# Kernel tuning notes

Measured on AMD Instinct MI355X. Metric: run time of the kernel, lower is better.

The kernel has to match this reference:

```python
import jax, jax.numpy as jnp
import numpy as np

N = 20000
E = 640000
D = 128      # node_dim
R = 32       # rbf_dim
H = 128      # radial_hidden_dim
CUTOFF = 5.0
RES_SCALE_INIT = 0.1
LN_EPS = 1e-5


def _init_linear(key, fan_in, fan_out):
    kw, kb = jax.random.split(key)
    bound = 1.0 / np.sqrt(fan_in)
    w = jax.random.uniform(kw, (fan_in, fan_out), minval=-bound, maxval=bound, dtype=jnp.float32)
    b = jax.random.uniform(kb, (fan_out,), minval=-bound, maxval=bound, dtype=jnp.float32)
    return w, b


def setup_inputs() -> dict:
    key = jax.random.key(0)
    ks = jax.random.split(key, 16)
    x = jax.random.normal(ks[0], (N, D), dtype=jnp.float32)
    edge_src = jax.random.randint(ks[1], (E,), 0, N)
    edge_dst = jax.random.randint(ks[2], (E,), 0, N)
    edge_sh = jax.random.normal(ks[3], (E, 16), dtype=jnp.float32)
    edge_rbf = jax.random.uniform(ks[4], (E, R), dtype=jnp.float32)
    edge_len = jax.random.uniform(ks[5], (E,), dtype=jnp.float32) * 8.0  # some edges beyond cutoff

    wm_w1, wm_b1 = _init_linear(ks[6], R, H)
    wm_w2, wm_b2 = _init_linear(ks[7], H, H)
    wm_w3, wm_b3 = _init_linear(ks[8], H, D)
    eg_w1, eg_b1 = _init_linear(ks[9], R, H)
    eg_w2, eg_b2 = _init_linear(ks[10], H, 1)
    mm_w1, mm_b1 = _init_linear(ks[11], D, H)
    mm_w2, mm_b2 = _init_linear(ks[12], H, D)
    sl_w, sl_b = _init_linear(ks[13], D, D)
    ul_w, ul_b = _init_linear(ks[14], D, D)

    return {
        "x": x, "edge_src": edge_src, "edge_dst": edge_dst,
        "edge_sh": edge_sh, "edge_rbf": edge_rbf, "edge_len": edge_len,
        "ln_g": jnp.ones((D,), jnp.float32), "ln_b": jnp.zeros((D,), jnp.float32),
        "wm_w1": wm_w1, "wm_b1": wm_b1, "wm_w2": wm_w2, "wm_b2": wm_b2,
        "wm_w3": wm_w3, "wm_b3": wm_b3,
        "eg_w1": eg_w1, "eg_b1": eg_b1, "eg_w2": eg_w2, "eg_b2": eg_b2,
        "mm_w1": mm_w1, "mm_b1": mm_b1, "mm_w2": mm_w2, "mm_b2": mm_b2,
        "sl_w": sl_w, "sl_b": sl_b, "ul_w": ul_w, "ul_b": ul_b,
        "res_scale": jnp.float32(RES_SCALE_INIT),
    }


def reference(x, edge_src, edge_dst, edge_sh, edge_rbf, edge_len,
              ln_g, ln_b,
              wm_w1, wm_b1, wm_w2, wm_b2, wm_w3, wm_b3,
              eg_w1, eg_b1, eg_w2, eg_b2,
              mm_w1, mm_b1, mm_w2, mm_b2,
              sl_w, sl_b, ul_w, ul_b, res_scale):
    # pre-LayerNorm
    mu = jnp.mean(x, axis=-1, keepdims=True)
    var = jnp.var(x, axis=-1, keepdims=True)
    x_norm = (x - mu) * jax.lax.rsqrt(var + LN_EPS) * ln_g + ln_b  # [N, D]

    # cosine cutoff * sigmoid edge gate -> [E, 1]
    r = edge_len / CUTOFF
    cut = 0.5 * (jnp.cos(jnp.pi * r) + 1.0) * (edge_len <= CUTOFF).astype(x.dtype)
    g = jax.nn.silu(edge_rbf @ eg_w1 + eg_b1)
    gate = jax.nn.sigmoid(g @ eg_w2 + eg_b2)  # [E, 1]
    edge_w = cut[:, None] * gate               # [E, 1]

    # radial weight MLP [E, D]
    h = jax.nn.silu(edge_rbf @ wm_w1 + wm_b1)
    h = jax.nn.silu(h @ wm_w2 + wm_b2)
    w_rad = h @ wm_w3 + wm_b3

    # gather, gate, scatter-add
    m = x_norm[edge_src] * w_rad * edge_w       # [E, D]
    agg = jax.ops.segment_sum(m, edge_dst, num_segments=N)          # [N, D]
    norm = jax.ops.segment_sum(edge_w, edge_dst, num_segments=N)    # [N, 1]
    agg = agg / jnp.maximum(norm, 1e-8)

    # message MLP + update
    a = jax.nn.silu(agg @ mm_w1 + mm_b1)
    agg2 = a @ mm_w2 + mm_b2
    out = (x_norm @ sl_w + sl_b) + (agg2 @ ul_w + ul_b)
    return x + res_scale * out
```

## Files before the change

### kernel.cpp

```cpp
#include <hip/hip_runtime.h>
#include <math.h>

#define N_NODES 20000
#define N_EDGES 640000
#define DD 128
#define RR 32
#define HH 128
#define PI_F 3.14159265358979323846f

#define NPACK 416
#define NLN   5000
#define NHIST 2500

typedef short bf16x8 __attribute__((ext_vector_type(8)));
typedef float f32x4 __attribute__((ext_vector_type(4)));
typedef __bf16 bf16x2_t __attribute__((ext_vector_type(2)));

__device__ __forceinline__ float silu_f(float x) {
    return x * __builtin_amdgcn_rcpf(1.0f + __expf(-x));
}
__device__ __forceinline__ float sigmoid_f(float x) {
    return __builtin_amdgcn_rcpf(1.0f + __expf(-x));
}
__device__ __forceinline__ unsigned short f2bf(float x) {
    __bf16 h = (__bf16)x;
    return __builtin_bit_cast(unsigned short, h);
}
__device__ __forceinline__ unsigned pk2(float lo, float hi) {
    bf16x2_t v;
    v[0] = (__bf16)lo; v[1] = (__bf16)hi;
    return __builtin_bit_cast(unsigned, v);
}
__device__ __forceinline__ bf16x8 frag8(float4 a, float4 b) {
    union { unsigned u[4]; bf16x8 v; } r;
    r.u[0] = pk2(a.x, a.y); r.u[1] = pk2(a.z, a.w);
    r.u[2] = pk2(b.x, b.y); r.u[3] = pk2(b.z, b.w);
    return r.v;
}

__device__ __forceinline__ unsigned short pack_one(const float* __restrict__ src,
                                                   int o, int F) {
    int NT = F >> 4;
    int j = o & 7;
    int l = (o >> 3) & 63;
    int rest = o >> 9;
    int t = rest % NT;
    int s = rest / NT;
    int k = s * 32 + ((l >> 4) << 3) + j;
    int f = t * 16 + (l & 15);
    return f2bf(src[(size_t)k * F + f]);
}

__global__ __launch_bounds__(256) void prep_kernel(
    const float* __restrict__ eg_w1, const float* __restrict__ wm_w1,
    const float* __restrict__ wm_w2, const float* __restrict__ wm_w3,
    const float* __restrict__ mm_w1, const float* __restrict__ mm_w2,
    const float* __restrict__ sl_w,  const float* __restrict__ ul_w,
    unsigned short* __restrict__ wp,
    const float* __restrict__ x, const float* __restrict__ g,
    const float* __restrict__ b, float* __restrict__ xn,
    const int* __restrict__ edst, const float* __restrict__ elen,
    int* __restrict__ cnt)
{
    const int blk = blockIdx.x;
    if (blk < NPACK) {
        int o = blk * 256 + threadIdx.x;
        unsigned short v;
        if      (o < 4096)   v = pack_one(eg_w1, o,          HH);
        else if (o < 8192)   v = pack_one(wm_w1, o - 4096,   HH);
        else if (o < 24576)  v = pack_one(wm_w2, o - 8192,   HH);
        else if (o < 40960)  v = pack_one(wm_w3, o - 24576,  DD);
        else if (o < 57344)  v = pack_one(mm_w1, o - 40960,  HH);
        else if (o < 73728)  v = pack_one(mm_w2, o - 57344,  DD);
        else if (o < 90112)  v = pack_one(sl_w,  o - 73728,  DD);
        else                 v = pack_one(ul_w,  o - 90112,  DD);
        wp[o] = v;
    } else if (blk < NPACK + NLN) {
        int wid = ((blk - NPACK) * 256 + threadIdx.x) >> 6;
        int lane = threadIdx.x & 63;
        if (wid >= N_NODES) return;
        const float* row = x + (size_t)wid * DD;
        float v0 = row[lane], v1 = row[lane + 64];
        float s = v0 + v1, sq = v0 * v0 + v1 * v1;
        #pragma unroll
        for (int o = 32; o > 0; o >>= 1) { s += __shfl_xor(s, o); sq += __shfl_xor(sq, o); }
        float mu = s * (1.0f / 128.0f);
        float var = sq * (1.0f / 128.0f) - mu * mu;
        float inv = rsqrtf(var + 1e-5f);
        float* orow = xn + (size_t)wid * DD;
        orow[lane]      = (v0 - mu) * inv * g[lane]      + b[lane];
        orow[lane + 64] = (v1 - mu) * inv * g[lane + 64] + b[lane + 64];
    } else {
        int e = (blk - NPACK - NLN) * 256 + threadIdx.x;
        if (e < N_EDGES && elen[e] <= 5.0f) atomicAdd(&cnt[edst[e]], 1);
    }
}

__global__ __launch_bounds__(1024) void scan_kernel(const int* __restrict__ cnt,
                                                    int* __restrict__ offs,
                                                    int* __restrict__ cursor) {
    __shared__ int part[1024];
    const int t = threadIdx.x;
    const int per = 20;
    const int base = t * per;
    int s = 0;
    for (int i = 0; i < per; ++i) {
        int idx = base + i;
        if (idx < N_NODES) s += cnt[idx];
    }
    part[t] = s;
    __syncthreads();
    for (int off = 1; off < 1024; off <<= 1) {
        int v = (t >= off) ? part[t - off] : 0;
        __syncthreads();
        part[t] += v;
        __syncthreads();
    }
    int run = part[t] - s;
    for (int i = 0; i < per; ++i) {
        int idx = base + i;
        if (idx < N_NODES) {
            offs[idx] = run;
            cursor[idx] = run;
            run += cnt[idx];
        }
    }
    if (t == 1023) offs[N_NODES] = part[1023];
}

__global__ __launch_bounds__(256) void fill_kernel(const int* __restrict__ esrc,
                                                   const int* __restrict__ edst,
                                                   const float* __restrict__ elen,
                                                   int* __restrict__ cursor,
                                                   int4* __restrict__ erec) {
    int e = blockIdx.x * 256 + threadIdx.x;
    if (e >= N_EDGES) return;
    float len = elen[e];
    if (len <= 5.0f) {
        int d = edst[e];
        int pos = atomicAdd(&cursor[d], 1);
        float cut = 0.5f * (__cosf(PI_F * len * 0.2f) + 1.0f);
        int4 rec;
        rec.x = e;
        rec.y = esrc[e];
        rec.z = d;
        rec.w = __float_as_int(cut);
        erec[pos] = rec;
    }
}

__global__ __launch_bounds__(256, 4) void edge_seg_kernel(
    const float* __restrict__ xn,
    const float* __restrict__ rbf,
    const int4* __restrict__ erec, const int* __restrict__ nlive_p,
    const unsigned short* __restrict__ wp_eg1, const unsigned short* __restrict__ wp_w1,
    const unsigned short* __restrict__ wp_w2,  const unsigned short* __restrict__ wp_w3,
    const float* __restrict__ eg_b1, const float* __restrict__ eg_w2,
    const float* __restrict__ eg_b2,
    const float* __restrict__ wm_b1, const float* __restrict__ wm_b2,
    const float* __restrict__ wm_b3,
    float* __restrict__ agg, float* __restrict__ nrm)
{
    __shared__ unsigned short act[4][32 * 136];
    __shared__ float ew_s[128];
    __shared__ int   dst_s[128];

    const int nlive = nlive_p[0];
    if (blockIdx.x * 128 >= nlive) return;

    const int tid  = threadIdx.x;
    const int w    = tid >> 6;
    const int lane = tid & 63;
    const int er   = lane & 15;
    const int kq   = lane >> 4;

    const int g0 = blockIdx.x * 128 + w * 32 + er;
    const int g1 = g0 + 16;
    const bool v0 = g0 < nlive, v1 = g1 < nlive;
    const int4 r0 = erec[v0 ? g0 : nlive - 1];
    const int4 r1 = erec[v1 ? g1 : nlive - 1];

    const int e0 = r0.x, src0 = r0.y, dst0 = r0.z;
    const int e1 = r1.x, src1 = r1.y, dst1 = r1.z;
    const float cut0 = v0 ? __int_as_float(r0.w) : 0.0f;
    const float cut1 = v1 ? __int_as_float(r1.w) : 0.0f;

    const float4* rp = (const float4*)(rbf + (size_t)e0 * RR + kq * 8);
    bf16x8 bfr0 = frag8(rp[0], rp[1]);
    const float4* rq = (const float4*)(rbf + (size_t)e1 * RR + kq * 8);
    bf16x8 bfr1 = frag8(rq[0], rq[1]);

    unsigned short* buf = &act[w][0];

    float pd0 = 0.0f, pd1 = 0.0f;
    {
        bf16x8 agc = *(const bf16x8*)(wp_eg1 + (size_t)lane * 8);
        bf16x8 a1c = *(const bf16x8*)(wp_w1  + (size_t)lane * 8);
        #pragma unroll
        for (int t = 0; t < 8; ++t) {
            const int tn = (t + 1) & 7;
            bf16x8 agn = *(const bf16x8*)(wp_eg1 + ((size_t)tn * 64 + lane) * 8);
            bf16x8 a1n = *(const bf16x8*)(wp_w1  + ((size_t)tn * 64 + lane) * 8);
            float4 gb = *(const float4*)(eg_b1 + t * 16 + kq * 4);
            float4 b1 = *(const float4*)(wm_b1 + t * 16 + kq * 4);
            f32x4 cg0 = {gb.x, gb.y, gb.z, gb.w};
            f32x4 cg1 = cg0;
            f32x4 c10 = {b1.x, b1.y, b1.z, b1.w};
            f32x4 c11 = c10;
            cg0 = __builtin_amdgcn_mfma_f32_16x16x32_bf16(agc, bfr0, cg0, 0, 0, 0);
            cg1 = __builtin_amdgcn_mfma_f32_16x16x32_bf16(agc, bfr1, cg1, 0, 0, 0);
            c10 = __builtin_amdgcn_mfma_f32_16x16x32_bf16(a1c, bfr0, c10, 0, 0, 0);
            c11 = __builtin_amdgcn_mfma_f32_16x16x32_bf16(a1c, bfr1, c11, 0, 0, 0);
            float4 w2 = *(const float4*)(eg_w2 + t * 16 + kq * 4);
            pd0 += silu_f(cg0[0])*w2.x + silu_f(cg0[1])*w2.y
                 + silu_f(cg0[2])*w2.z + silu_f(cg0[3])*w2.w;
            pd1 += silu_f(cg1[0])*w2.x + silu_f(cg1[1])*w2.y
                 + silu_f(cg1[2])*w2.z + silu_f(cg1[3])*w2.w;
            *(uint2*)(buf + er * 136 + t * 16 + kq * 4) =
                make_uint2(pk2(silu_f(c10[0]), silu_f(c10[1])),
                           pk2(silu_f(c10[2]), silu_f(c10[3])));
            *(uint2*)(buf + (16 + er) * 136 + t * 16 + kq * 4) =
                make_uint2(pk2(silu_f(c11[0]), silu_f(c11[1])),
                           pk2(silu_f(c11[2]), silu_f(c11[3])));
            agc = agn; a1c = a1n;
        }
    }
    pd0 += __shfl_xor(pd0, 16); pd0 += __shfl_xor(pd0, 32);
    pd1 += __shfl_xor(pd1, 16); pd1 += __shfl_xor(pd1, 32);
    const float eb2 = eg_b2[0];
    const float ew0 = cut0 * sigmoid_f(pd0 + eb2);
    const float ew1 = cut1 * sigmoid_f(pd1 + eb2);
    if (lane < 16) {
        ew_s[w * 32 + er] = ew0;       dst_s[w * 32 + er] = dst0;
        ew_s[w * 32 + 16 + er] = ew1;  dst_s[w * 32 + 16 + er] = dst1;
    }

    bf16x8 h0[4], h1[4];
    #pragma unroll
    for (int s = 0; s < 4; ++s) {
        h0[s] = *(const bf16x8*)(buf + er * 136 + s * 32 + kq * 8);
        h1[s] = *(const bf16x8*)(buf + (16 + er) * 136 + s * 32 + kq * 8);
    }
    {
        bf16x8 afc[4];
        #pragma unroll
        for (int s = 0; s < 4; ++s)
            afc[s] = *(const bf16x8*)(wp_w2 + ((size_t)(s * 8) * 64 + lane) * 8);
        #pragma unroll
        for (int t = 0; t < 8; ++t) {
            const int tn = (t + 1) & 7;
            bf16x8 afn[4];
            #pragma unroll
            for (int s = 0; s < 4; ++s)
                afn[s] = *(const bf16x8*)(wp_w2 + (((size_t)s * 8 + tn) * 64 + lane) * 8);
            float4 b2 = *(const float4*)(wm_b2 + t * 16 + kq * 4);
            f32x4 a0 = {b2.x, b2.y, b2.z, b2.w}, b0 = {0.f, 0.f, 0.f, 0.f};
            f32x4 a1 = a0, b1v = {0.f, 0.f, 0.f, 0.f};
            a0 = __builtin_amdgcn_mfma_f32_16x16x32_bf16(afc[0], h0[0], a0, 0, 0, 0);
            b0 = __builtin_amdgcn_mfma_f32_16x16x32_bf16(afc[2], h0[2], b0, 0, 0, 0);
            a1 = __builtin_amdgcn_mfma_f32_16x16x32_bf16(afc[0], h1[0], a1, 0, 0, 0);
            b1v = __builtin_amdgcn_mfma_f32_16x16x32_bf16(afc[2], h1[2], b1v, 0, 0, 0);
            a0 = __builtin_amdgcn_mfma_f32_16x16x32_bf16(afc[1], h0[1], a0, 0, 0, 0);
            b0 = __builtin_amdgcn_mfma_f32_16x16x32_bf16(afc[3], h0[3], b0, 0, 0, 0);
            a1 = __builtin_amdgcn_mfma_f32_16x16x32_bf16(afc[1], h1[1], a1, 0, 0, 0);
            b1v = __builtin_amdgcn_mfma_f32_16x16x32_bf16(afc[3], h1[3], b1v, 0, 0, 0);
            f32x4 c0 = a0 + b0;
            f32x4 c1 = a1 + b1v;
            *(uint2*)(buf + er * 136 + t * 16 + kq * 4) =
                make_uint2(pk2(silu_f(c0[0]), silu_f(c0[1])),
                           pk2(silu_f(c0[2]), silu_f(c0[3])));
            *(uint2*)(buf + (16 + er) * 136 + t * 16 + kq * 4) =
                make_uint2(pk2(silu_f(c1[0]), silu_f(c1[1])),
                           pk2(silu_f(c1[2]), silu_f(c1[3])));
            #pragma unroll
            for (int s = 0; s < 4; ++s) afc[s] = afn[s];
        }
    }

    #pragma unroll
    for (int s = 0; s < 4; ++s) {
        h0[s] = *(const bf16x8*)(buf + er * 136 + s * 32 + kq * 8);
        h1[s] = *(const bf16x8*)(buf + (16 + er) * 136 + s * 32 + kq * 8);
    }
    const float* xr0 = xn + (size_t)src0 * DD;
    const float* xr1 = xn + (size_t)src1 * DD;
    {
        bf16x8 afc[4];
        #pragma unroll
        for (int s = 0; s < 4; ++s)
            afc[s] = *(const bf16x8*)(wp_w3 + ((size_t)(s * 8) * 64 + lane) * 8);
        #pragma unroll
        for (int t = 0; t < 8; ++t) {
            const int tn = (t + 1) & 7;
            bf16x8 afn[4];
            #pragma unroll
            for (int s = 0; s < 4; ++s)
                afn[s] = *(const bf16x8*)(wp_w3 + (((size_t)s * 8 + tn) * 64 + lane) * 8);
            float4 b3 = *(const float4*)(wm_b3 + t * 16 + kq * 4);
            f32x4 a0 = {b3.x, b3.y, b3.z, b3.w}, b0 = {0.f, 0.f, 0.f, 0.f};
            f32x4 a1 = a0, b1v = {0.f, 0.f, 0.f, 0.f};
            a0 = __builtin_amdgcn_mfma_f32_16x16x32_bf16(afc[0], h0[0], a0, 0, 0, 0);
            b0 = __builtin_amdgcn_mfma_f32_16x16x32_bf16(afc[2], h0[2], b0, 0, 0, 0);
            a1 = __builtin_amdgcn_mfma_f32_16x16x32_bf16(afc[0], h1[0], a1, 0, 0, 0);
            b1v = __builtin_amdgcn_mfma_f32_16x16x32_bf16(afc[2], h1[2], b1v, 0, 0, 0);
            a0 = __builtin_amdgcn_mfma_f32_16x16x32_bf16(afc[1], h0[1], a0, 0, 0, 0);
            b0 = __builtin_amdgcn_mfma_f32_16x16x32_bf16(afc[3], h0[3], b0, 0, 0, 0);
            a1 = __builtin_amdgcn_mfma_f32_16x16x32_bf16(afc[1], h1[1], a1, 0, 0, 0);
            b1v = __builtin_amdgcn_mfma_f32_16x16x32_bf16(afc[3], h1[3], b1v, 0, 0, 0);
            f32x4 c0 = a0 + b0;
            f32x4 c1 = a1 + b1v;
            float4 xv0 = *(const float4*)(xr0 + t * 16 + kq * 4);
            float4 xv1 = *(const float4*)(xr1 + t * 16 + kq * 4);
            *(uint2*)(buf + er * 136 + t * 16 + kq * 4) =
                make_uint2(pk2(c0[0]*xv0.x*ew0, c0[1]*xv0.y*ew0),
                           pk2(c0[2]*xv0.z*ew0, c0[3]*xv0.w*ew0));
            *(uint2*)(buf + (16 + er) * 136 + t * 16 + kq * 4) =
                make_uint2(pk2(c1[0]*xv1.x*ew1, c1[1]*xv1.y*ew1),
                           pk2(c1[2]*xv1.z*ew1, c1[3]*xv1.w*ew1));
            #pragma unroll
            for (int s = 0; s < 4; ++s) afc[s] = afn[s];
        }
    }

    {
        const int rb = w * 32;
        float run0 = 0.0f, run1 = 0.0f, ewrun = 0.0f;
        int cur = dst_s[rb];
        #pragma unroll 8
        for (int i = 0; i < 32; ++i) {
            const int d = dst_s[rb + i];
            if (d != cur) {
                atomicAdd(&agg[(size_t)cur * DD + 2 * lane], run0);
                atomicAdd(&agg[(size_t)cur * DD + 2 * lane + 1], run1);
                if (lane == 0) atomicAdd(&nrm[cur], ewrun);
                run0 = 0.0f; run1 = 0.0f; ewrun = 0.0f; cur = d;
            }
            unsigned pv = *(const unsigned*)(buf + i * 136 + 2 * lane);
            run0 += __uint_as_float(pv << 16);
            run1 += __uint_as_float(pv & 0xffff0000u);
            ewrun += ew_s[rb + i];
        }
        atomicAdd(&agg[(size_t)cur * DD + 2 * lane], run0);
        atomicAdd(&agg[(size_t)cur * DD + 2 * lane + 1], run1);
        if (lane == 0) atomicAdd(&nrm[cur], ewrun);
    }
}

__global__ __launch_bounds__(256) void node_kernel(
    const float* __restrict__ x, const float* __restrict__ xn,
    const float* __restrict__ agg, const float* __restrict__ nrm,
    const unsigned short* __restrict__ wp_mm1, const unsigned short* __restrict__ wp_mm2,
    const unsigned short* __restrict__ wp_sl,  const unsigned short* __restrict__ wp_ul,
    const float* __restrict__ mm_b1, const float* __restrict__ mm_b2,
    const float* __restrict__ sl_b, const float* __restrict__ ul_b,
    const float* __restrict__ res_scale, float* __restrict__ out)
{
    __shared__ unsigned short act[4][16 * 136];

    const int tid  = threadIdx.x;
    const int w    = tid >> 6;
    const int lane = tid & 63;
    const int er   = lane & 15;
    const int kq   = lane >> 4;

    const int n0 = blockIdx.x * 64 + w * 16 + er;
    const bool val0 = n0 < N_NODES;
    const int nc0 = val0 ? n0 : N_NODES - 1;

    const float rs0 = __builtin_amdgcn_rcpf(fmaxf(nrm[nc0], 1e-8f));
    const float rscl = res_scale[0];

    bf16x8 ba0[4];
    #pragma unroll
    for (int s = 0; s < 4; ++s) {
        const float4* ap = (const float4*)(agg + (size_t)nc0 * DD + s * 32 + kq * 8);
        float4 a = ap[0], b = ap[1];
        a.x*=rs0; a.y*=rs0; a.z*=rs0; a.w*=rs0; b.x*=rs0; b.y*=rs0; b.z*=rs0; b.w*=rs0;
        ba0[s] = frag8(a, b);
    }

    unsigned short* buf = &act[w][0];

    #pragma unroll
    for (int t = 0; t < 8; ++t) {
        float4 b1 = *(const float4*)(mm_b1 + t * 16 + kq * 4);
        f32x4 c0 = {b1.x, b1.y, b1.z, b1.w};
        #pragma unroll
        for (int s = 0; s < 4; ++s) {
            bf16x8 af = *(const bf16x8*)(wp_mm1 + (((size_t)s * 8 + t) * 64 + lane) * 8);
            c0 = __builtin_amdgcn_mfma_f32_16x16x32_bf16(af, ba0[s], c0, 0, 0, 0);
        }
        *(uint2*)(buf + er * 136 + t * 16 + kq * 4) =
            make_uint2(pk2(silu_f(c0[0]), silu_f(c0[1])),
                       pk2(silu_f(c0[2]), silu_f(c0[3])));
    }

    bf16x8 bh0[4];
    #pragma unroll
    for (int s = 0; s < 4; ++s)
        bh0[s] = *(const bf16x8*)(buf + er * 136 + s * 32 + kq * 8);
    #pragma unroll
    for (int t = 0; t < 8; ++t) {
        float4 b2 = *(const float4*)(mm_b2 + t * 16 + kq * 4);
        f32x4 c0 = {b2.x, b2.y, b2.z, b2.w};
        #pragma unroll
        for (int s = 0; s < 4; ++s) {
            bf16x8 af = *(const bf16x8*)(wp_mm2 + (((size_t)s * 8 + t) * 64 + lane) * 8);
            c0 = __builtin_amdgcn_mfma_f32_16x16x32_bf16(af, bh0[s], c0, 0, 0, 0);
        }
        *(uint2*)(buf + er * 136 + t * 16 + kq * 4) =
            make_uint2(pk2(c0[0], c0[1]), pk2(c0[2], c0[3]));
    }

    bf16x8 bg0[4], bx0[4];
    #pragma unroll
    for (int s = 0; s < 4; ++s) {
        bg0[s] = *(const bf16x8*)(buf + er * 136 + s * 32 + kq * 8);
        const float4* xp = (const float4*)(xn + (size_t)nc0 * DD + s * 32 + kq * 8);
        bx0[s] = frag8(xp[0], xp[1]);
    }

    #pragma unroll
    for (int t = 0; t < 8; ++t) {
        float4 sb = *(const float4*)(sl_b + t * 16 + kq * 4);
        float4 ub = *(const float4*)(ul_b + t * 16 + kq * 4);
        f32x4 c0 = {sb.x + ub.x, sb.y + ub.y, sb.z + ub.z, sb.w + ub.w};
        #pragma unroll
        for (int s = 0; s < 4; ++s) {
            bf16x8 af = *(const bf16x8*)(wp_sl + (((size_t)s * 8 + t) * 64 + lane) * 8);
            c0 = __builtin_amdgcn_mfma_f32_16x16x32_bf16(af, bx0[s], c0, 0, 0, 0);
        }
        #pragma unroll
        for (int s = 0; s < 4; ++s) {
            bf16x8 af = *(const bf16x8*)(wp_ul + (((size_t)s * 8 + t) * 64 + lane) * 8);
            c0 = __builtin_amdgcn_mfma_f32_16x16x32_bf16(af, bg0[s], c0, 0, 0, 0);
        }
        if (val0) {
            float4 xv = *(const float4*)(x + (size_t)n0 * DD + t * 16 + kq * 4);
            float4 o;
            o.x = xv.x + rscl * c0[0];
            o.y = xv.y + rscl * c0[1];
            o.z = xv.z + rscl * c0[2];
            o.w = xv.w + rscl * c0[3];
            *(float4*)(out + (size_t)n0 * DD + t * 16 + kq * 4) = o;
        }
    }
}

extern "C" void kernel_launch(void* const* d_in, const int* in_sizes, int n_in,
                              void* d_out, int out_size, void* d_ws, size_t ws_size,
                              hipStream_t stream) {
    const float* x     = (const float*)d_in[0];
    const int*   esrc  = (const int*)d_in[1];
    const int*   edst  = (const int*)d_in[2];
    const float* rbf   = (const float*)d_in[4];
    const float* elen  = (const float*)d_in[5];
    const float* ln_g  = (const float*)d_in[6];
    const float* ln_b  = (const float*)d_in[7];
    const float* wm_w1 = (const float*)d_in[8];
    const float* wm_b1 = (const float*)d_in[9];
    const float* wm_w2 = (const float*)d_in[10];
    const float* wm_b2 = (const float*)d_in[11];
    const float* wm_w3 = (const float*)d_in[12];
    const float* wm_b3 = (const float*)d_in[13];
    const float* eg_w1 = (const float*)d_in[14];
    const float* eg_b1 = (const float*)d_in[15];
    const float* eg_w2 = (const float*)d_in[16];
    const float* eg_b2 = (const float*)d_in[17];
    const float* mm_w1 = (const float*)d_in[18];
    const float* mm_b1 = (const float*)d_in[19];
    const float* mm_w2 = (const float*)d_in[20];
    const float* mm_b2 = (const float*)d_in[21];
    const float* sl_w  = (const float*)d_in[22];
    const float* sl_b  = (const float*)d_in[23];
    const float* ul_w  = (const float*)d_in[24];
    const float* ul_b  = (const float*)d_in[25];
    const float* rscl  = (const float*)d_in[26];

    float* xn  = (float*)d_ws;
    float* agg = xn + (size_t)N_NODES * DD;
    float* nrm = agg + (size_t)N_NODES * DD;
    int*   cnt = (int*)(nrm + N_NODES);
    unsigned short* wp = (unsigned short*)(cnt + N_NODES);
    unsigned short* wp_eg1 = wp;
    unsigned short* wp_w1  = wp + 4096;
    unsigned short* wp_w2  = wp + 8192;
    unsigned short* wp_w3  = wp + 24576;
    unsigned short* wp_mm1 = wp + 40960;
    unsigned short* wp_mm2 = wp + 57344;
    unsigned short* wp_sl  = wp + 73728;
    unsigned short* wp_ul  = wp + 90112;
    int* offs   = (int*)(wp + 106496);
    int* cursor = offs + N_NODES + 1;
    int4* erec  = (int4*)(((size_t)(cursor + N_NODES) + 15) & ~(size_t)15);

    hipMemsetAsync(agg, 0, (size_t)(N_NODES * DD + 2 * N_NODES) * sizeof(float), stream);
    prep_kernel<<<NPACK + NLN + NHIST, 256, 0, stream>>>(
        eg_w1, wm_w1, wm_w2, wm_w3, mm_w1, mm_w2, sl_w, ul_w, wp,
        x, ln_g, ln_b, xn, edst, elen, cnt);
    scan_kernel<<<1, 1024, 0, stream>>>(cnt, offs, cursor);
    fill_kernel<<<N_EDGES / 256, 256, 0, stream>>>(esrc, edst, elen, cursor, erec);
    edge_seg_kernel<<<N_EDGES / 128, 256, 0, stream>>>(xn, rbf, erec, offs + N_NODES,
        wp_eg1, wp_w1, wp_w2, wp_w3,
        eg_b1, eg_w2, eg_b2, wm_b1, wm_b2, wm_b3, agg, nrm);
    node_kernel<<<(N_NODES + 63) / 64, 256, 0, stream>>>(x, xn, agg, nrm,
        wp_mm1, wp_mm2, wp_sl, wp_ul,
        mm_b1, mm_b2, sl_b, ul_b, rscl, (float*)d_out);
}
```

Before: 204.9 us.

## Fold agg zeroing into prep kernel and software-pipeline node-kernel weight loads

```diff
diff --git a/kernel.cpp b/kernel.cpp
--- a/kernel.cpp
+++ b/kernel.cpp
@@ -11,6 +11,7 @@
 #define NPACK 416
 #define NLN   5000
 #define NHIST 2500
+#define NZERO 2520
 
 typedef short bf16x8 __attribute__((ext_vector_type(8)));
 typedef float f32x4 __attribute__((ext_vector_type(4)));
@@ -60,7 +61,7 @@
     const float* __restrict__ x, const float* __restrict__ g,
     const float* __restrict__ b, float* __restrict__ xn,
     const int* __restrict__ edst, const float* __restrict__ elen,
-    int* __restrict__ cnt)
+    int* __restrict__ cnt, float4* __restrict__ aggz)
 {
     const int blk = blockIdx.x;
     if (blk < NPACK) {
@@ -90,9 +91,13 @@
         float* orow = xn + (size_t)wid * DD;
         orow[lane]      = (v0 - mu) * inv * g[lane]      + b[lane];
         orow[lane + 64] = (v1 - mu) * inv * g[lane + 64] + b[lane + 64];
-    } else {
+    } else if (blk < NPACK + NLN + NHIST) {
         int e = (blk - NPACK - NLN) * 256 + threadIdx.x;
         if (e < N_EDGES && elen[e] <= 5.0f) atomicAdd(&cnt[edst[e]], 1);
+    } else {
+        int i = (blk - NPACK - NLN - NHIST) * 256 + threadIdx.x;
+        if (i < (N_NODES * DD + N_NODES) / 4)
+            aggz[i] = make_float4(0.f, 0.f, 0.f, 0.f);
     }
 }
 
@@ -381,35 +386,61 @@
 
     unsigned short* buf = &act[w][0];
 
-    #pragma unroll
-    for (int t = 0; t < 8; ++t) {
-        float4 b1 = *(const float4*)(mm_b1 + t * 16 + kq * 4);
-        f32x4 c0 = {b1.x, b1.y, b1.z, b1.w};
-        #pragma unroll
-        for (int s = 0; s < 4; ++s) {
-            bf16x8 af = *(const bf16x8*)(wp_mm1 + (((size_t)s * 8 + t) * 64 + lane) * 8);
-            c0 = __builtin_amdgcn_mfma_f32_16x16x32_bf16(af, ba0[s], c0, 0, 0, 0);
-        }
-        *(uint2*)(buf + er * 136 + t * 16 + kq * 4) =
-            make_uint2(pk2(silu_f(c0[0]), silu_f(c0[1])),
-                       pk2(silu_f(c0[2]), silu_f(c0[3])));
+    {
+        bf16x8 afc[4];
+        #pragma unroll
+        for (int s = 0; s < 4; ++s)
+            afc[s] = *(const bf16x8*)(wp_mm1 + ((size_t)(s * 8) * 64 + lane) * 8);
+        #pragma unroll
+        for (int t = 0; t < 8; ++t) {
+            const int tn = (t + 1) & 7;
+            bf16x8 afn[4];
+            #pragma unroll
+            for (int s = 0; s < 4; ++s)
+                afn[s] = *(const bf16x8*)(wp_mm1 + (((size_t)s * 8 + tn) * 64 + lane) * 8);
+            float4 b1 = *(const float4*)(mm_b1 + t * 16 + kq * 4);
+            f32x4 ca = {b1.x, b1.y, b1.z, b1.w}, cb = {0.f, 0.f, 0.f, 0.f};
+            ca = __builtin_amdgcn_mfma_f32_16x16x32_bf16(afc[0], ba0[0], ca, 0, 0, 0);
+            cb = __builtin_amdgcn_mfma_f32_16x16x32_bf16(afc[2], ba0[2], cb, 0, 0, 0);
+            ca = __builtin_amdgcn_mfma_f32_16x16x32_bf16(afc[1], ba0[1], ca, 0, 0, 0);
+            cb = __builtin_amdgcn_mfma_f32_16x16x32_bf16(afc[3], ba0[3], cb, 0, 0, 0);
+            f32x4 c0 = ca + cb;
+            *(uint2*)(buf + er * 136 + t * 16 + kq * 4) =
+                make_uint2(pk2(silu_f(c0[0]), silu_f(c0[1])),
+                           pk2(silu_f(c0[2]), silu_f(c0[3])));
+            #pragma unroll
+            for (int s = 0; s < 4; ++s) afc[s] = afn[s];
+        }
     }
 
     bf16x8 bh0[4];
     #pragma unroll
     for (int s = 0; s < 4; ++s)
         bh0[s] = *(const bf16x8*)(buf + er * 136 + s * 32 + kq * 8);
-    #pragma unroll
-    for (int t = 0; t < 8; ++t) {
-        float4 b2 = *(const float4*)(mm_b2 + t * 16 + kq * 4);
-        f32x4 c0 = {b2.x, b2.y, b2.z, b2.w};
-        #pragma unroll
-        for (int s = 0; s < 4; ++s) {
-            bf16x8 af = *(const bf16x8*)(wp_mm2 + (((size_t)s * 8 + t) * 64 + lane) * 8);
-            c0 = __builtin_amdgcn_mfma_f32_16x16x32_bf16(af, bh0[s], c0, 0, 0, 0);
-        }
-        *(uint2*)(buf + er * 136 + t * 16 + kq * 4) =
-            make_uint2(pk2(c0[0], c0[1]), pk2(c0[2], c0[3]));
+    {
+        bf16x8 afc[4];
+        #pragma unroll
+        for (int s = 0; s < 4; ++s)
+            afc[s] = *(const bf16x8*)(wp_mm2 + ((size_t)(s * 8) * 64 + lane) * 8);
+        #pragma unroll
+        for (int t = 0; t < 8; ++t) {
+            const int tn = (t + 1) & 7;
+            bf16x8 afn[4];
+            #pragma unroll
+            for (int s = 0; s < 4; ++s)
+                afn[s] = *(const bf16x8*)(wp_mm2 + (((size_t)s * 8 + tn) * 64 + lane) * 8);
+            float4 b2 = *(const float4*)(mm_b2 + t * 16 + kq * 4);
+            f32x4 ca = {b2.x, b2.y, b2.z, b2.w}, cb = {0.f, 0.f, 0.f, 0.f};
+            ca = __builtin_amdgcn_mfma_f32_16x16x32_bf16(afc[0], bh0[0], ca, 0, 0, 0);
+            cb = __builtin_amdgcn_mfma_f32_16x16x32_bf16(afc[2], bh0[2], cb, 0, 0, 0);
+            ca = __builtin_amdgcn_mfma_f32_16x16x32_bf16(afc[1], bh0[1], ca, 0, 0, 0);
+            cb = __builtin_amdgcn_mfma_f32_16x16x32_bf16(afc[3], bh0[3], cb, 0, 0, 0);
+            f32x4 c0 = ca + cb;
+            *(uint2*)(buf + er * 136 + t * 16 + kq * 4) =
+                make_uint2(pk2(c0[0], c0[1]), pk2(c0[2], c0[3]));
+            #pragma unroll
+            for (int s = 0; s < 4; ++s) afc[s] = afn[s];
+        }
     }
 
     bf16x8 bg0[4], bx0[4];
@@ -420,29 +451,45 @@
         bx0[s] = frag8(xp[0], xp[1]);
     }
 
-    #pragma unroll
-    for (int t = 0; t < 8; ++t) {
-        float4 sb = *(const float4*)(sl_b + t * 16 + kq * 4);
-        float4 ub = *(const float4*)(ul_b + t * 16 + kq * 4);
-        f32x4 c0 = {sb.x + ub.x, sb.y + ub.y, sb.z + ub.z, sb.w + ub.w};
+    {
+        bf16x8 slc[4], ulc[4];
         #pragma unroll
         for (int s = 0; s < 4; ++s) {
-            bf16x8 af = *(const bf16x8*)(wp_sl + (((size_t)s * 8 + t) * 64 + lane) * 8);
-            c0 = __builtin_amdgcn_mfma_f32_16x16x32_bf16(af, bx0[s], c0, 0, 0, 0);
-        }
-        #pragma unroll
-        for (int s = 0; s < 4; ++s) {
-            bf16x8 af = *(const bf16x8*)(wp_ul + (((size_t)s * 8 + t) * 64 + lane) * 8);
-            c0 = __builtin_amdgcn_mfma_f32_16x16x32_bf16(af, bg0[s], c0, 0, 0, 0);
-        }
-        if (val0) {
-            float4 xv = *(const float4*)(x + (size_t)n0 * DD + t * 16 + kq * 4);
-            float4 o;
-            o.x = xv.x + rscl * c0[0];
-            o.y = xv.y + rscl * c0[1];
-            o.z = xv.z + rscl * c0[2];
-            o.w = xv.w + rscl * c0[3];
-            *(float4*)(out + (size_t)n0 * DD + t * 16 + kq * 4) = o;
+            slc[s] = *(const bf16x8*)(wp_sl + ((size_t)(s * 8) * 64 + lane) * 8);
+            ulc[s] = *(const bf16x8*)(wp_ul + ((size_t)(s * 8) * 64 + lane) * 8);
+        }
+        #pragma unroll
+        for (int t = 0; t < 8; ++t) {
+            const int tn = (t + 1) & 7;
+            bf16x8 sln[4], uln[4];
+            #pragma unroll
+            for (int s = 0; s < 4; ++s) {
+                sln[s] = *(const bf16x8*)(wp_sl + (((size_t)s * 8 + tn) * 64 + lane) * 8);
+                uln[s] = *(const bf16x8*)(wp_ul + (((size_t)s * 8 + tn) * 64 + lane) * 8);
+            }
+            float4 sb = *(const float4*)(sl_b + t * 16 + kq * 4);
+            float4 ub = *(const float4*)(ul_b + t * 16 + kq * 4);
+            f32x4 cs = {sb.x + ub.x, sb.y + ub.y, sb.z + ub.z, sb.w + ub.w};
+            f32x4 cu = {0.f, 0.f, 0.f, 0.f};
+            cs = __builtin_amdgcn_mfma_f32_16x16x32_bf16(slc[0], bx0[0], cs, 0, 0, 0);
+            cu = __builtin_amdgcn_mfma_f32_16x16x32_bf16(ulc[0], bg0[0], cu, 0, 0, 0);
+            cs = __builtin_amdgcn_mfma_f32_16x16x32_bf16(slc[1], bx0[1], cs, 0, 0, 0);
+            cu = __builtin_amdgcn_mfma_f32_16x16x32_bf16(ulc[1], bg0[1], cu, 0, 0, 0);
+            cs = __builtin_amdgcn_mfma_f32_16x16x32_bf16(slc[2], bx0[2], cs, 0, 0, 0);
+            cu = __builtin_amdgcn_mfma_f32_16x16x32_bf16(ulc[2], bg0[2], cu, 0, 0, 0);
+            cs = __builtin_amdgcn_mfma_f32_16x16x32_bf16(slc[3], bx0[3], cs, 0, 0, 0);
+            cu = __builtin_amdgcn_mfma_f32_16x16x32_bf16(ulc[3], bg0[3], cu, 0, 0, 0);
+            if (val0) {
+                float4 xv = *(const float4*)(x + (size_t)n0 * DD + t * 16 + kq * 4);
+                float4 o;
+                o.x = xv.x + rscl * (cs[0] + cu[0]);
+                o.y = xv.y + rscl * (cs[1] + cu[1]);
+                o.z = xv.z + rscl * (cs[2] + cu[2]);
+                o.w = xv.w + rscl * (cs[3] + cu[3]);
+                *(float4*)(out + (size_t)n0 * DD + t * 16 + kq * 4) = o;
+            }
+            #pragma unroll
+            for (int s = 0; s < 4; ++s) { slc[s] = sln[s]; ulc[s] = uln[s]; }
         }
     }
 }
@@ -494,10 +541,10 @@
     int* cursor = offs + N_NODES + 1;
     int4* erec  = (int4*)(((size_t)(cursor + N_NODES) + 15) & ~(size_t)15);
 
-    hipMemsetAsync(agg, 0, (size_t)(N_NODES * DD + 2 * N_NODES) * sizeof(float), stream);
-    prep_kernel<<<NPACK + NLN + NHIST, 256, 0, stream>>>(
+    hipMemsetAsync(cnt, 0, (size_t)N_NODES * sizeof(int), stream);
+    prep_kernel<<<NPACK + NLN + NHIST + NZERO, 256, 0, stream>>>(
         eg_w1, wm_w1, wm_w2, wm_w3, mm_w1, mm_w2, sl_w, ul_w, wp,
-        x, ln_g, ln_b, xn, edst, elen, cnt);
+        x, ln_g, ln_b, xn, edst, elen, cnt, (float4*)agg);
     scan_kernel<<<1, 1024, 0, stream>>>(cnt, offs, cursor);
     fill_kernel<<<N_EDGES / 256, 256, 0, stream>>>(esrc, edst, elen, cursor, erec);
     edge_seg_kernel<<<N_EDGES / 128, 256, 0, stream>>>(xn, rbf, erec, offs + N_NODES,
```

Result: no change. 203.3 us (median of 2 runs) (-0.8%).
